# Kernel optimization log

Hardware: AMD Instinct MI355X
Metric: run time of the kernel (lower is better)

The kernel has to match this reference:

```python
import jax, jax.numpy as jnp
import numpy as np

N = 50000
E = 800000
F_IN = 300
ALPHA = 0.5                      # GCN2Conv alpha
BETA = float(np.log(0.2 / 2.0 + 1.0))  # log(theta/layer + 1), theta=0.2, layer=2
NEG_SLOPE = 0.2                  # GATv2 leaky_relu slope
H, DH = 2, 32                    # GATv2 heads, per-head dim


def _glorot(key, shape):
    s = (6.0 / (shape[0] + shape[-1])) ** 0.5
    return jax.random.uniform(key, shape, jnp.float32, -s, s)


def setup_inputs() -> dict:
    key = jax.random.key(0)
    ks = jax.random.split(key, 24)
    inp = {
        'x': jax.random.normal(ks[0], (N, F_IN), jnp.float32),
        'edge_index': jax.random.randint(ks[1], (2, E), 0, N, dtype=jnp.int32),
        # encoder params
        'W_enc1': _glorot(ks[2], (F_IN, 256)), 'b_enc1': jnp.zeros((256,), jnp.float32),
        'W_enc2': _glorot(ks[3], (256, 256)),                       # GCN2Conv (no bias)
        'W_enc3': _glorot(ks[4], (256, 128)), 'b_enc3': jnp.zeros((128,), jnp.float32),
        'W_enc4': _glorot(ks[5], (128, 64)),  'b_enc4': jnp.zeros((64,), jnp.float32),
        'W_enc5': _glorot(ks[6], (64, 32)),   'b_enc5': jnp.zeros((32,), jnp.float32),
        'Wl_gat': _glorot(ks[7], (32, H * DH)),
        'Wr_gat': _glorot(ks[8], (32, H * DH)),
        'att_gat': _glorot(ks[9], (H, DH)),
        'b_gat': jnp.zeros((H * DH,), jnp.float32),
        # decoder params
        'W_dec1': _glorot(ks[10], (64, 128)),  'b_dec1': jnp.zeros((128,), jnp.float32),
        'W_dec2': _glorot(ks[11], (128, 256)), 'b_dec2': jnp.zeros((256,), jnp.float32),
        'W_dec3': _glorot(ks[12], (256, 256)),                      # GCN2Conv (no bias)
        'W_dec4': _glorot(ks[13], (256, F_IN)), 'b_dec4': jnp.zeros((F_IN,), jnp.float32),
    }
    return inp


def _forward(x, edge_index,
             W_enc1, b_enc1, W_enc2, W_enc3, b_enc3, W_enc4, b_enc4, W_enc5, b_enc5,
             Wl_gat, Wr_gat, att_gat, b_gat,
             W_dec1, b_dec1, W_dec2, b_dec2, W_dec3, W_dec4, b_dec4):
    loops = jnp.arange(N, dtype=edge_index.dtype)
    src = jnp.concatenate([edge_index[0], loops])  # [E+N]
    dst = jnp.concatenate([edge_index[1], loops])
    # symmetric GCN normalization with self-loops (PyG gcn_norm)
    deg = jax.ops.segment_sum(jnp.ones_like(src, jnp.float32), dst, num_segments=N)
    dinv = jnp.where(deg > 0, jax.lax.rsqrt(jnp.maximum(deg, 1e-12)), 0.0)
    norm = dinv[src] * dinv[dst]  # [E+N]

    def prop(h):  # normalized adjacency apply: gather -> scale -> scatter-add
        return jax.ops.segment_sum(h[src] * norm[:, None], dst, num_segments=N)

    def gcn(h, W, b):
        return prop(h @ W) + b

    def gcn2(h, W):  # GCNII with x_0 = layer input, shared weights
        hp = (1.0 - ALPHA) * prop(h) + ALPHA * h
        return (1.0 - BETA) * hp + BETA * (hp @ W)

    def gatv2(h, Wl, Wr, att, b):
        xl = (h @ Wl).reshape(N, H, DH)  # source transform
        xr = (h @ Wr).reshape(N, H, DH)  # target transform
        e = jax.nn.leaky_relu(xl[src] + xr[dst], NEG_SLOPE)  # [E+N, H, DH]
        logits = jnp.einsum('ehd,hd->eh', e, att)            # [E+N, H]
        m = jax.lax.stop_gradient(jax.ops.segment_max(logits, dst, num_segments=N))
        ex = jnp.exp(logits - m[dst])
        den = jax.ops.segment_sum(ex, dst, num_segments=N)
        a = ex / (den[dst] + 1e-16)                          # softmax over in-edges
        out = jax.ops.segment_sum(xl[src] * a[:, :, None], dst, num_segments=N)
        return out.reshape(N, H * DH) + b

    h = gcn(x, W_enc1, b_enc1)
    h = gcn2(h, W_enc2)
    h = gcn(h, W_enc3, b_enc3)
    h = gcn(h, W_enc4, b_enc4)
    h = gcn(h, W_enc5, b_enc5)
    h = gatv2(h, Wl_gat, Wr_gat, att_gat, b_gat)
    h = jax.nn.relu(h)
    h = gcn(h, W_dec1, b_dec1)
    h = gcn(h, W_dec2, b_dec2)
    h = gcn2(h, W_dec3)
    h = gcn(h, W_dec4, b_dec4)
    return jax.nn.sigmoid(h)


def reference(x, edge_index,
              W_enc1, b_enc1, W_enc2, W_enc3, b_enc3, W_enc4, b_enc4, W_enc5, b_enc5,
              Wl_gat, Wr_gat, att_gat, b_gat,
              W_dec1, b_dec1, W_dec2, b_dec2, W_dec3, W_dec4, b_dec4):
    return _forward(x, edge_index,
                    W_enc1, b_enc1, W_enc2, W_enc3, b_enc3, W_enc4, b_enc4, W_enc5, b_enc5,
                    Wl_gat, Wr_gat, att_gat, b_gat,
                    W_dec1, b_dec1, W_dec2, b_dec2, W_dec3, W_dec4, b_dec4)
```

## Files before the change

### kernel.cpp

```cpp
#include <hip/hip_runtime.h>
#include <math.h>

#define NN 50000
#define FIN 300
#define SS 304
constexpr float ALPHA_C = 0.5f;
constexpr float BETA_C  = 0.09531017980432486f;
constexpr float NEG_SLOPE = 0.2f;

typedef unsigned short u16;
typedef __attribute__((ext_vector_type(8))) short short8;
typedef __attribute__((ext_vector_type(4))) float f32x4;
typedef _Float16 hf4 __attribute__((ext_vector_type(4)));

__global__ void hist_kernel(const int* __restrict__ dst, int* __restrict__ deg, int E) {
    int e = blockIdx.x * blockDim.x + threadIdx.x;
    if (e < E) atomicAdd(&deg[dst[e]], 1);
}

__global__ void scan_kernel(const int* __restrict__ deg, int* __restrict__ rowptr, int n) {
    __shared__ int sh[1024];
    __shared__ int carry;
    if (threadIdx.x == 0) { carry = 0; rowptr[0] = 0; }
    __syncthreads();
    for (int base = 0; base < n; base += 1024) {
        int i = base + threadIdx.x;
        int v = (i < n) ? deg[i] : 0;
        sh[threadIdx.x] = v;
        __syncthreads();
        for (int off = 1; off < 1024; off <<= 1) {
            int t = (threadIdx.x >= off) ? sh[threadIdx.x - off] : 0;
            __syncthreads();
            sh[threadIdx.x] += t;
            __syncthreads();
        }
        if (i < n) rowptr[i + 1] = sh[threadIdx.x] + carry;
        __syncthreads();
        if (threadIdx.x == 0) carry += sh[1023];
        __syncthreads();
    }
}

__global__ void dinv_kernel(const int* __restrict__ deg, float* __restrict__ dinv, int n) {
    int i = blockIdx.x * blockDim.x + threadIdx.x;
    if (i < n) dinv[i] = rsqrtf((float)deg[i] + 1.0f);
}

__global__ void copy_int_kernel(const int* __restrict__ a, int* __restrict__ b, int n) {
    int i = blockIdx.x * blockDim.x + threadIdx.x;
    if (i < n) b[i] = a[i];
}

__global__ void fill_kernel(const int* __restrict__ src, const int* __restrict__ dst,
                            const float* __restrict__ dinv, int* __restrict__ cursor,
                            int* __restrict__ csr_src, float* __restrict__ csr_w, int E) {
    int e = blockIdx.x * blockDim.x + threadIdx.x;
    if (e < E) {
        int s = src[e], d = dst[e];
        int p = atomicAdd(&cursor[d], 1);
        csr_src[p] = s;
        csr_w[p]   = dinv[s] * dinv[d];
    }
}

__global__ void splitw_kernel(const float* __restrict__ W, u16* __restrict__ WhT,
                              u16* __restrict__ WlT, int K, int M, int Kp, int total) {
    int t = blockIdx.x * blockDim.x + threadIdx.x;
    if (t >= total) return;
    int c = t / Kp, k = t - c * Kp;
    float x = (c < M && k < K) ? W[(size_t)k * M + c] : 0.f;
    unsigned u = __float_as_uint(x);
    WhT[t] = (u16)(u >> 16);
    float lo = x - __uint_as_float(u & 0xFFFF0000u);
    WlT[t] = (u16)(__float_as_uint(lo) >> 16);
}

__global__ __launch_bounds__(256)
void gemm_mfma_kernel(const float* __restrict__ A, const u16* __restrict__ WhT,
                      const u16* __restrict__ WlT, float* __restrict__ C,
                      _Float16* __restrict__ Cs, int n, int K, int M, int Kp,
                      float cAB, float cA, const float* __restrict__ bias, int gx) {
    __shared__ u16 sAh[64 * 40], sAl[64 * 40], sWh[64 * 40], sWl[64 * 40];
    const int tid = threadIdx.x;
    const int nwg = gridDim.x;
    const int q = nwg >> 3, r = nwg & 7;
    const int xcd = blockIdx.x & 7, off = blockIdx.x >> 3;
    const int wgid = (xcd < r ? xcd * (q + 1) : r * (q + 1) + (xcd - r) * q) + off;
    const int colBase = (wgid % gx) * 64;
    const int rowBase = (wgid / gx) * 64;
    const int lane = tid & 63, wid = tid >> 6;
    const int wr = (wid >> 1) * 32, wc = (wid & 1) * 32;
    const int fr = lane & 15, ko = (lane >> 4) * 8;
    const int wsc = tid >> 2, wsk = (tid & 3) * 8;

    f32x4 acc[2][2] = {};

    for (int k0 = 0; k0 < Kp; k0 += 32) {
        {
            size_t g = (size_t)(colBase + wsc) * Kp + k0 + wsk;
            *(uint4*)&sWh[wsc * 40 + wsk] = *(const uint4*)&WhT[g];
            *(uint4*)&sWl[wsc * 40 + wsk] = *(const uint4*)&WlT[g];
        }
        const bool fullk = (k0 + 32 <= K);
        for (int s = tid; s < 512; s += 256) {
            int rr = s >> 3, kb = (s & 7) * 4;
            int gr = rowBase + rr, kk = k0 + kb;
            float x0 = 0.f, x1 = 0.f, x2 = 0.f, x3 = 0.f;
            if (gr < n) {
                const float* ap = A + (size_t)gr * K + kk;
                if (fullk) { float4 v = *(const float4*)ap; x0 = v.x; x1 = v.y; x2 = v.z; x3 = v.w; }
                else {
                    if (kk     < K) x0 = ap[0];
                    if (kk + 1 < K) x1 = ap[1];
                    if (kk + 2 < K) x2 = ap[2];
                    if (kk + 3 < K) x3 = ap[3];
                }
            }
            unsigned u0 = __float_as_uint(x0), u1 = __float_as_uint(x1);
            unsigned u2 = __float_as_uint(x2), u3 = __float_as_uint(x3);
            uint2 hp; hp.x = (u1 & 0xFFFF0000u) | (u0 >> 16);
                      hp.y = (u3 & 0xFFFF0000u) | (u2 >> 16);
            float l0 = x0 - __uint_as_float(u0 & 0xFFFF0000u);
            float l1 = x1 - __uint_as_float(u1 & 0xFFFF0000u);
            float l2 = x2 - __uint_as_float(u2 & 0xFFFF0000u);
            float l3 = x3 - __uint_as_float(u3 & 0xFFFF0000u);
            uint2 lp; lp.x = (__float_as_uint(l1) & 0xFFFF0000u) | (__float_as_uint(l0) >> 16);
                      lp.y = (__float_as_uint(l3) & 0xFFFF0000u) | (__float_as_uint(l2) >> 16);
            *(uint2*)&sAh[rr * 40 + kb] = hp;
            *(uint2*)&sAl[rr * 40 + kb] = lp;
        }
        __syncthreads();

        short8 ah[2], al[2], bh[2], bl[2];
        ah[0] = *(const short8*)&sAh[(wr +      fr) * 40 + ko];
        ah[1] = *(const short8*)&sAh[(wr + 16 + fr) * 40 + ko];
        al[0] = *(const short8*)&sAl[(wr +      fr) * 40 + ko];
        al[1] = *(const short8*)&sAl[(wr + 16 + fr) * 40 + ko];
        bh[0] = *(const short8*)&sWh[(wc +      fr) * 40 + ko];
        bh[1] = *(const short8*)&sWh[(wc + 16 + fr) * 40 + ko];
        bl[0] = *(const short8*)&sWl[(wc +      fr) * 40 + ko];
        bl[1] = *(const short8*)&sWl[(wc + 16 + fr) * 40 + ko];
#pragma unroll
        for (int i = 0; i < 2; i++)
#pragma unroll
            for (int j = 0; j < 2; j++) {
                acc[i][j] = __builtin_amdgcn_mfma_f32_16x16x32_bf16(al[i], bh[j], acc[i][j], 0, 0, 0);
                acc[i][j] = __builtin_amdgcn_mfma_f32_16x16x32_bf16(ah[i], bl[j], acc[i][j], 0, 0, 0);
                acc[i][j] = __builtin_amdgcn_mfma_f32_16x16x32_bf16(ah[i], bh[j], acc[i][j], 0, 0, 0);
            }
        __syncthreads();
    }

#pragma unroll
    for (int i = 0; i < 2; i++)
#pragma unroll
        for (int j = 0; j < 2; j++) {
            int row0 = rowBase + wr + i * 16 + (lane >> 4) * 4;
            int col  = colBase + wc + j * 16 + fr;
            if (col >= M) continue;
            float bv = bias ? bias[col] : 0.f;
#pragma unroll
            for (int qq = 0; qq < 4; qq++) {
                int rr = row0 + qq;
                if (rr >= n) break;
                float v = cAB * acc[i][j][qq] + bv;
                if (cA != 0.f) v += cA * A[(size_t)rr * K + col];
                C[(size_t)rr * M + col] = v;
                if (Cs) Cs[(size_t)rr * SS + col] = (_Float16)v;
            }
        }
}

__global__ __launch_bounds__(256)
void prop_kernel(const float* __restrict__ h, const _Float16* __restrict__ hs,
                 float* __restrict__ out, _Float16* __restrict__ outs,
                 const int* __restrict__ rowptr, const int* __restrict__ csr_src,
                 const float* __restrict__ csr_w, const float* __restrict__ dinv,
                 const float* __restrict__ bias, int n, int D, float cP, float cH) {
    int wv = (blockIdx.x * blockDim.x + threadIdx.x) >> 6;
    int lane = threadIdx.x & 63;
    int D4 = D >> 2;
    int npw = 64 / D4;
    int sub = lane / D4;
    int cl = lane - sub * D4;
    int i = wv * npw + sub;
    if (i >= n) return;
    int c = cl * 4;
    long bi = (long)i * D4 + cl;
    const float4* h4 = (const float4*)h;
    float4 hv = h4[bi];
    float sw = dinv[i] * dinv[i];
    float4 a0 = {sw * hv.x, sw * hv.y, sw * hv.z, sw * hv.w};
    float4 a1 = {0,0,0,0}, a2 = {0,0,0,0}, a3 = {0,0,0,0};
    int p0 = rowptr[i], p1 = rowptr[i + 1];
    int p = p0;
    for (; p + 4 <= p1; p += 4) {
        int s0 = csr_src[p], s1 = csr_src[p+1], s2 = csr_src[p+2], s3 = csr_src[p+3];
        float w0 = csr_w[p], w1 = csr_w[p+1], w2 = csr_w[p+2], w3 = csr_w[p+3];
        hf4 v0 = *(const hf4*)&hs[(size_t)s0 * SS + c];
        hf4 v1 = *(const hf4*)&hs[(size_t)s1 * SS + c];
        hf4 v2 = *(const hf4*)&hs[(size_t)s2 * SS + c];
        hf4 v3 = *(const hf4*)&hs[(size_t)s3 * SS + c];
        a0.x += w0*(float)v0[0]; a0.y += w0*(float)v0[1]; a0.z += w0*(float)v0[2]; a0.w += w0*(float)v0[3];
        a1.x += w1*(float)v1[0]; a1.y += w1*(float)v1[1]; a1.z += w1*(float)v1[2]; a1.w += w1*(float)v1[3];
        a2.x += w2*(float)v2[0]; a2.y += w2*(float)v2[1]; a2.z += w2*(float)v2[2]; a2.w += w2*(float)v2[3];
        a3.x += w3*(float)v3[0]; a3.y += w3*(float)v3[1]; a3.z += w3*(float)v3[2]; a3.w += w3*(float)v3[3];
    }
    for (; p < p1; ++p) {
        int s = csr_src[p];
        float w = csr_w[p];
        hf4 v = *(const hf4*)&hs[(size_t)s * SS + c];
        a0.x += w*(float)v[0]; a0.y += w*(float)v[1]; a0.z += w*(float)v[2]; a0.w += w*(float)v[3];
    }
    float4 acc = {a0.x + a1.x + a2.x + a3.x, a0.y + a1.y + a2.y + a3.y,
                  a0.z + a1.z + a2.z + a3.z, a0.w + a1.w + a2.w + a3.w};
    float4 rr = {cP * acc.x, cP * acc.y, cP * acc.z, cP * acc.w};
    if (cH != 0.f) { rr.x += cH * hv.x; rr.y += cH * hv.y; rr.z += cH * hv.z; rr.w += cH * hv.w; }
    if (bias) { float4 b = ((const float4*)bias)[cl]; rr.x += b.x; rr.y += b.y; rr.z += b.z; rr.w += b.w; }
    ((float4*)out)[bi] = rr;
    if (outs) {
        hf4 o; o[0] = (_Float16)rr.x; o[1] = (_Float16)rr.y; o[2] = (_Float16)rr.z; o[3] = (_Float16)rr.w;
        *(hf4*)&outs[(size_t)i * SS + c] = o;
    }
}

__device__ inline float lrelu(float x) { return x > 0.f ? x : NEG_SLOPE * x; }

__global__ __launch_bounds__(256)
void gat_logits_kernel(const float* __restrict__ xl, const _Float16* __restrict__ xls,
                       const float* __restrict__ xr, const float* __restrict__ att,
                       const int* __restrict__ rowptr, const int* __restrict__ csr_src,
                       float* __restrict__ logits, float* __restrict__ self_logits, int n) {
    int t = blockIdx.x * blockDim.x + threadIdx.x;
    int i = t >> 1, hh = t & 1;
    if (i >= n) return;
    float4 attv[8], xrv[8];
    const float4* att4 = (const float4*)att;
    const float4* xr4 = (const float4*)xr;
#pragma unroll
    for (int c = 0; c < 8; c++) {
        attv[c] = att4[hh * 8 + c];
        xrv[c]  = xr4[(long)i * 16 + hh * 8 + c];
    }
    {
        const float4* xl4 = (const float4*)xl;
        float s = 0.f;
        long b = (long)i * 16 + hh * 8;
#pragma unroll
        for (int c = 0; c < 8; c++) {
            float4 e = xl4[b + c];
            s += lrelu(e.x + xrv[c].x) * attv[c].x;
            s += lrelu(e.y + xrv[c].y) * attv[c].y;
            s += lrelu(e.z + xrv[c].z) * attv[c].z;
            s += lrelu(e.w + xrv[c].w) * attv[c].w;
        }
        self_logits[i * 2 + hh] = s;
    }
    int p0 = rowptr[i], p1 = rowptr[i + 1];
    for (int p = p0; p < p1; ++p) {
        int sn = csr_src[p];
        size_t b = (size_t)sn * SS + hh * 32;
        float s = 0.f;
#pragma unroll
        for (int c = 0; c < 8; c++) {
            hf4 e = *(const hf4*)&xls[b + c * 4];
            s += lrelu((float)e[0] + xrv[c].x) * attv[c].x;
            s += lrelu((float)e[1] + xrv[c].y) * attv[c].y;
            s += lrelu((float)e[2] + xrv[c].z) * attv[c].z;
            s += lrelu((float)e[3] + xrv[c].w) * attv[c].w;
        }
        logits[(long)p * 2 + hh] = s;
    }
}

__global__ __launch_bounds__(256)
void gat_mden_kernel(const float* __restrict__ logits, const float* __restrict__ self_logits,
                     const int* __restrict__ rowptr, float* __restrict__ m_arr,
                     float* __restrict__ den_arr, int n) {
    int t = blockIdx.x * blockDim.x + threadIdx.x;
    int i = t >> 1, hh = t & 1;
    if (i >= n) return;
    int p0 = rowptr[i], p1 = rowptr[i + 1];
    float m = self_logits[i * 2 + hh];
    for (int p = p0; p < p1; ++p) m = fmaxf(m, logits[(long)p * 2 + hh]);
    float den = expf(self_logits[i * 2 + hh] - m);
    for (int p = p0; p < p1; ++p) den += expf(logits[(long)p * 2 + hh] - m);
    m_arr[i * 2 + hh] = m;
    den_arr[i * 2 + hh] = den;
}

__global__ __launch_bounds__(256)
void gat_out_kernel(const float* __restrict__ xl, const _Float16* __restrict__ xls,
                    const int* __restrict__ rowptr, const int* __restrict__ csr_src,
                    const float* __restrict__ logits, const float* __restrict__ self_logits,
                    const float* __restrict__ m_arr, const float* __restrict__ den_arr,
                    const float* __restrict__ bias, float* __restrict__ out,
                    _Float16* __restrict__ outs, int n) {
    int i = (blockIdx.x * blockDim.x + threadIdx.x) >> 6;
    int lane = threadIdx.x & 63;
    if (i >= n) return;
    int hh = lane >> 5;
    float m = m_arr[i * 2 + hh];
    float inv = 1.f / (den_arr[i * 2 + hh] + 1e-16f);
    float acc = expf(self_logits[i * 2 + hh] - m) * inv * xl[(long)i * 64 + lane];
    int p0 = rowptr[i], p1 = rowptr[i + 1];
    for (int p = p0; p < p1; ++p) {
        float w = expf(logits[(long)p * 2 + hh] - m) * inv;
        acc += w * (float)xls[(size_t)csr_src[p] * SS + lane];
    }
    float r = fmaxf(acc + bias[lane], 0.f);
    out[(long)i * 64 + lane] = r;
    outs[(size_t)i * SS + lane] = (_Float16)r;
}

__global__ void sigmoid_kernel(const float* __restrict__ in, float* __restrict__ out, int n4) {
    int i = blockIdx.x * blockDim.x + threadIdx.x;
    if (i < n4) {
        float4 v = ((const float4*)in)[i];
        float4 r;
        r.x = 1.f / (1.f + expf(-v.x));
        r.y = 1.f / (1.f + expf(-v.y));
        r.z = 1.f / (1.f + expf(-v.z));
        r.w = 1.f / (1.f + expf(-v.w));
        ((float4*)out)[i] = r;
    }
}

extern "C" void kernel_launch(void* const* d_in, const int* in_sizes, int n_in,
                              void* d_out, int out_size, void* d_ws, size_t ws_size,
                              hipStream_t stream) {
    const int N = NN;
    const int E = in_sizes[1] / 2;

    struct WSpec { int idx; int K, M; };
    const WSpec wspec[11] = {
        {2, 300, 256},
        {4, 256, 256},
        {5, 256, 128},
        {7, 128, 64},
        {9, 64, 32},
        {11, 32, 64},
        {12, 32, 64},
        {15, 64, 128},
        {17, 128, 256},
        {19, 256, 256},
        {20, 256, 300},
    };
    size_t arena_elems = 0;
    int kp[11], mp[11];
    size_t woff[11];
    for (int i = 0; i < 11; i++) {
        kp[i] = (wspec[i].K + 31) & ~31;
        mp[i] = (wspec[i].M + 63) & ~63;
        woff[i] = arena_elems;
        arena_elems += (size_t)2 * mp[i] * kp[i];
    }

    size_t need = 0;
    need += (size_t)N * 304 * 4 * 2;
    need += (size_t)N * SS * 2;
    need += (size_t)E * 4;
    need += (size_t)E * 2 * 4;
    need += (size_t)N * 2 * 4 * 3;
    need += (size_t)N * 4;
    need += (size_t)N * 4;
    need += (size_t)(N + 4) * 4;
    need += (size_t)N * 4;
    need += (size_t)E * 4;
    need += arena_elems * 2 + 128;
    if (ws_size < need) return;

    const float* x      = (const float*)d_in[0];
    const int*   ei     = (const int*)d_in[1];
    const int*   e_src  = ei;
    const int*   e_dst  = ei + E;
    const float* b1  = (const float*)d_in[3];
    const float* b3  = (const float*)d_in[6];
    const float* b4  = (const float*)d_in[8];
    const float* b5  = (const float*)d_in[10];
    const float* attw= (const float*)d_in[13];
    const float* bg  = (const float*)d_in[14];
    const float* bd1 = (const float*)d_in[16];
    const float* bd2 = (const float*)d_in[18];
    const float* bd4 = (const float*)d_in[21];

    char* w = (char*)d_ws;
    float* bufA = (float*)w;                 w += (size_t)N * 304 * 4;
    float* bufB = (float*)w;                 w += (size_t)N * 304 * 4;
    _Float16* S = (_Float16*)w;              w += (size_t)N * SS * 2;
    float* csr_w = (float*)w;                w += (size_t)E * 4;
    float* logits = (float*)w;               w += (size_t)E * 2 * 4;
    float* self_logits = (float*)w;          w += (size_t)N * 2 * 4;
    float* m_arr = (float*)w;                w += (size_t)N * 2 * 4;
    float* den_arr = (float*)w;              w += (size_t)N * 2 * 4;
    float* dinv = (float*)w;                 w += (size_t)N * 4;
    int* deg = (int*)w;                      w += (size_t)N * 4;
    int* rowptr = (int*)w;                   w += (size_t)(N + 4) * 4;
    int* cursor = (int*)w;                   w += (size_t)N * 4;
    int* csr_src = (int*)w;                  w += (size_t)E * 4;
    w = (char*)(((size_t)w + 63) & ~(size_t)63);
    u16* arena = (u16*)w;                    w += arena_elems * 2;
    float* T = (float*)d_out;

    int nb_e = (E + 255) / 256;
    int nb_n = (N + 255) / 256;
    int nb_wave = (N + 3) / 4;
    int nb_2n = (2 * N + 255) / 256;

    for (int i = 0; i < 11; i++) {
        int total = mp[i] * kp[i];
        splitw_kernel<<<(total + 255) / 256, 256, 0, stream>>>(
            (const float*)d_in[wspec[i].idx], arena + woff[i], arena + woff[i] + total,
            wspec[i].K, wspec[i].M, kp[i], total);
    }

    hipMemsetAsync(deg, 0, (size_t)N * 4, stream);
    hist_kernel<<<nb_e, 256, 0, stream>>>(e_dst, deg, E);
    scan_kernel<<<1, 1024, 0, stream>>>(deg, rowptr, N);
    dinv_kernel<<<nb_n, 256, 0, stream>>>(deg, dinv, N);
    copy_int_kernel<<<nb_n, 256, 0, stream>>>(rowptr, cursor, N);
    fill_kernel<<<nb_e, 256, 0, stream>>>(e_src, e_dst, dinv, cursor, csr_src, csr_w, E);

    auto gemm = [&](int wi, const float* A, float* C, float cAB, float cA,
                    const float* bias, bool shadow) {
        int K = wspec[wi].K, M = wspec[wi].M;
        int total = mp[wi] * kp[wi];
        int gx = (M + 63) / 64, gy = (N + 63) / 64;
        gemm_mfma_kernel<<<gx * gy, 256, 0, stream>>>(
            A, arena + woff[wi], arena + woff[wi] + total, C, shadow ? S : nullptr,
            N, K, M, kp[wi], cAB, cA, bias, gx);
    };
    auto prop = [&](const float* h, float* out, int D, float cP, float cH,
                    const float* bias, bool shadow) {
        int npw = 64 / (D >> 2);
        int npb = 4 * npw;
        int nb = (N + npb - 1) / npb;
        prop_kernel<<<nb, 256, 0, stream>>>(h, S, out, shadow ? S : nullptr,
                                            rowptr, csr_src, csr_w, dinv,
                                            bias, N, D, cP, cH);
    };

    gemm(0, x, T, 1.f, 0.f, nullptr, true);
    prop(T, bufA, 256, 1.f, 0.f, b1, true);
    prop(bufA, bufB, 256, 1.f - ALPHA_C, ALPHA_C, nullptr, false);
    gemm(1, bufB, bufA, BETA_C, 1.f - BETA_C, nullptr, false);
    gemm(2, bufA, T, 1.f, 0.f, nullptr, true);
    prop(T, bufB, 128, 1.f, 0.f, b3, false);
    gemm(3, bufB, T, 1.f, 0.f, nullptr, true);
    prop(T, bufA, 64, 1.f, 0.f, b4, false);
    gemm(4, bufA, T, 1.f, 0.f, nullptr, true);
    prop(T, bufB, 32, 1.f, 0.f, b5, false);
    gemm(5, bufB, bufA, 1.f, 0.f, nullptr, true);
    gemm(6, bufB, T, 1.f, 0.f, nullptr, false);
    gat_logits_kernel<<<nb_2n, 256, 0, stream>>>(bufA, S, T, attw, rowptr, csr_src,
                                                 logits, self_logits, N);
    gat_mden_kernel<<<nb_2n, 256, 0, stream>>>(logits, self_logits, rowptr, m_arr, den_arr, N);
    gat_out_kernel<<<nb_wave, 256, 0, stream>>>(bufA, S, rowptr, csr_src, logits, self_logits,
                                                m_arr, den_arr, bg, bufB, S, N);
    prop(bufB, bufA, 64, 1.f, 0.f, nullptr, false);
    gemm(7, bufA, T, 1.f, 0.f, bd1, true);
    prop(T, bufB, 128, 1.f, 0.f, nullptr, false);
    gemm(8, bufB, bufA, 1.f, 0.f, bd2, true);
    prop(bufA, bufB, 256, 1.f - ALPHA_C, ALPHA_C, nullptr, false);
    gemm(9, bufB, bufA, BETA_C, 1.f - BETA_C, nullptr, true);
    prop(bufA, bufB, 256, 1.f, 0.f, nullptr, false);
    gemm(10, bufB, T, 1.f, 0.f, bd4, false);
    sigmoid_kernel<<<(out_size / 4 + 255) / 256, 256, 0, stream>>>(T, (float*)d_out, out_size / 4);
}
```

Measured before the change: 1.326 ms.

## Switch activations to fp16 storage and use split-weight f16 MFMA GEMMs

```diff
diff --git a/kernel.cpp b/kernel.cpp
--- a/kernel.cpp
+++ b/kernel.cpp
@@ -3,15 +3,16 @@
 
 #define NN 50000
 #define FIN 300
-#define SS 304
+#define SHS 256
+#define XS  320
 constexpr float ALPHA_C = 0.5f;
 constexpr float BETA_C  = 0.09531017980432486f;
 constexpr float NEG_SLOPE = 0.2f;
 
 typedef unsigned short u16;
-typedef __attribute__((ext_vector_type(8))) short short8;
 typedef __attribute__((ext_vector_type(4))) float f32x4;
 typedef _Float16 hf4 __attribute__((ext_vector_type(4)));
+typedef _Float16 half8 __attribute__((ext_vector_type(8)));
 
 __global__ void hist_kernel(const int* __restrict__ dst, int* __restrict__ deg, int E) {
     int e = blockIdx.x * blockDim.x + threadIdx.x;
@@ -63,24 +64,31 @@
     }
 }
 
-__global__ void splitw_kernel(const float* __restrict__ W, u16* __restrict__ WhT,
-                              u16* __restrict__ WlT, int K, int M, int Kp, int total) {
+__global__ void cvt_x_kernel(const float* __restrict__ x, _Float16* __restrict__ FX, int total) {
+    int t = blockIdx.x * blockDim.x + threadIdx.x;
+    if (t >= total) return;
+    int i = t / XS, c = t - i * XS;
+    FX[t] = (c < FIN) ? (_Float16)x[(size_t)i * FIN + c] : (_Float16)0.f;
+}
+
+__global__ void splitw_kernel(const float* __restrict__ W, _Float16* __restrict__ WhT,
+                              _Float16* __restrict__ WlT, int K, int M, int Kp, int total) {
     int t = blockIdx.x * blockDim.x + threadIdx.x;
     if (t >= total) return;
     int c = t / Kp, k = t - c * Kp;
     float x = (c < M && k < K) ? W[(size_t)k * M + c] : 0.f;
-    unsigned u = __float_as_uint(x);
-    WhT[t] = (u16)(u >> 16);
-    float lo = x - __uint_as_float(u & 0xFFFF0000u);
-    WlT[t] = (u16)(__float_as_uint(lo) >> 16);
+    _Float16 hi = (_Float16)x;
+    WhT[t] = hi;
+    WlT[t] = (_Float16)(x - (float)hi);
 }
 
 __global__ __launch_bounds__(256)
-void gemm_mfma_kernel(const float* __restrict__ A, const u16* __restrict__ WhT,
-                      const u16* __restrict__ WlT, float* __restrict__ C,
-                      _Float16* __restrict__ Cs, int n, int K, int M, int Kp,
-                      float cAB, float cA, const float* __restrict__ bias, int gx) {
-    __shared__ u16 sAh[64 * 40], sAl[64 * 40], sWh[64 * 40], sWl[64 * 40];
+void gemm_f16_kernel(const _Float16* __restrict__ A, int lda,
+                     const _Float16* __restrict__ WhT, const _Float16* __restrict__ WlT,
+                     float* __restrict__ Cf, _Float16* __restrict__ Co,
+                     int n, int Kl, int M,
+                     float cAB, float cA, const float* __restrict__ bias, int gx) {
+    __shared__ _Float16 sA[64 * 40], sWh[64 * 40], sWl[64 * 40];
     const int tid = threadIdx.x;
     const int nwg = gridDim.x;
     const int q = nwg >> 3, r = nwg & 7;
@@ -92,61 +100,37 @@
     const int wr = (wid >> 1) * 32, wc = (wid & 1) * 32;
     const int fr = lane & 15, ko = (lane >> 4) * 8;
     const int wsc = tid >> 2, wsk = (tid & 3) * 8;
+    const int arr = tid >> 2, akq = (tid & 3) * 8;
 
     f32x4 acc[2][2] = {};
 
-    for (int k0 = 0; k0 < Kp; k0 += 32) {
+    for (int k0 = 0; k0 < Kl; k0 += 32) {
         {
-            size_t g = (size_t)(colBase + wsc) * Kp + k0 + wsk;
+            size_t g = (size_t)(colBase + wsc) * Kl + k0 + wsk;
             *(uint4*)&sWh[wsc * 40 + wsk] = *(const uint4*)&WhT[g];
             *(uint4*)&sWl[wsc * 40 + wsk] = *(const uint4*)&WlT[g];
         }
-        const bool fullk = (k0 + 32 <= K);
-        for (int s = tid; s < 512; s += 256) {
-            int rr = s >> 3, kb = (s & 7) * 4;
-            int gr = rowBase + rr, kk = k0 + kb;
-            float x0 = 0.f, x1 = 0.f, x2 = 0.f, x3 = 0.f;
-            if (gr < n) {
-                const float* ap = A + (size_t)gr * K + kk;
-                if (fullk) { float4 v = *(const float4*)ap; x0 = v.x; x1 = v.y; x2 = v.z; x3 = v.w; }
-                else {
-                    if (kk     < K) x0 = ap[0];
-                    if (kk + 1 < K) x1 = ap[1];
-                    if (kk + 2 < K) x2 = ap[2];
-                    if (kk + 3 < K) x3 = ap[3];
-                }
-            }
-            unsigned u0 = __float_as_uint(x0), u1 = __float_as_uint(x1);
-            unsigned u2 = __float_as_uint(x2), u3 = __float_as_uint(x3);
-            uint2 hp; hp.x = (u1 & 0xFFFF0000u) | (u0 >> 16);
-                      hp.y = (u3 & 0xFFFF0000u) | (u2 >> 16);
-            float l0 = x0 - __uint_as_float(u0 & 0xFFFF0000u);
-            float l1 = x1 - __uint_as_float(u1 & 0xFFFF0000u);
-            float l2 = x2 - __uint_as_float(u2 & 0xFFFF0000u);
-            float l3 = x3 - __uint_as_float(u3 & 0xFFFF0000u);
-            uint2 lp; lp.x = (__float_as_uint(l1) & 0xFFFF0000u) | (__float_as_uint(l0) >> 16);
-                      lp.y = (__float_as_uint(l3) & 0xFFFF0000u) | (__float_as_uint(l2) >> 16);
-            *(uint2*)&sAh[rr * 40 + kb] = hp;
-            *(uint2*)&sAl[rr * 40 + kb] = lp;
+        {
+            int gr = rowBase + arr;
+            uint4 v = {0, 0, 0, 0};
+            if (gr < n) v = *(const uint4*)&A[(size_t)gr * lda + k0 + akq];
+            *(uint4*)&sA[arr * 40 + akq] = v;
         }
         __syncthreads();
 
-        short8 ah[2], al[2], bh[2], bl[2];
-        ah[0] = *(const short8*)&sAh[(wr +      fr) * 40 + ko];
-        ah[1] = *(const short8*)&sAh[(wr + 16 + fr) * 40 + ko];
-        al[0] = *(const short8*)&sAl[(wr +      fr) * 40 + ko];
-        al[1] = *(const short8*)&sAl[(wr + 16 + fr) * 40 + ko];
-        bh[0] = *(const short8*)&sWh[(wc +      fr) * 40 + ko];
-        bh[1] = *(const short8*)&sWh[(wc + 16 + fr) * 40 + ko];
-        bl[0] = *(const short8*)&sWl[(wc +      fr) * 40 + ko];
-        bl[1] = *(const short8*)&sWl[(wc + 16 + fr) * 40 + ko];
+        half8 av[2], bh[2], bl[2];
+        av[0] = *(const half8*)&sA[(wr +      fr) * 40 + ko];
+        av[1] = *(const half8*)&sA[(wr + 16 + fr) * 40 + ko];
+        bh[0] = *(const half8*)&sWh[(wc +      fr) * 40 + ko];
+        bh[1] = *(const half8*)&sWh[(wc + 16 + fr) * 40 + ko];
+        bl[0] = *(const half8*)&sWl[(wc +      fr) * 40 + ko];
+        bl[1] = *(const half8*)&sWl[(wc + 16 + fr) * 40 + ko];
 #pragma unroll
         for (int i = 0; i < 2; i++)
 #pragma unroll
             for (int j = 0; j < 2; j++) {
-                acc[i][j] = __builtin_amdgcn_mfma_f32_16x16x32_bf16(al[i], bh[j], acc[i][j], 0, 0, 0);
-                acc[i][j] = __builtin_amdgcn_mfma_f32_16x16x32_bf16(ah[i], bl[j], acc[i][j], 0, 0, 0);
-                acc[i][j] = __builtin_amdgcn_mfma_f32_16x16x32_bf16(ah[i], bh[j], acc[i][j], 0, 0, 0);
+                acc[i][j] = __builtin_amdgcn_mfma_f32_16x16x32_f16(av[i], bl[j], acc[i][j], 0, 0, 0);
+                acc[i][j] = __builtin_amdgcn_mfma_f32_16x16x32_f16(av[i], bh[j], acc[i][j], 0, 0, 0);
             }
         __syncthreads();
     }
@@ -164,16 +148,15 @@
                 int rr = row0 + qq;
                 if (rr >= n) break;
                 float v = cAB * acc[i][j][qq] + bv;
-                if (cA != 0.f) v += cA * A[(size_t)rr * K + col];
-                C[(size_t)rr * M + col] = v;
-                if (Cs) Cs[(size_t)rr * SS + col] = (_Float16)v;
+                if (cA != 0.f) v += cA * (float)A[(size_t)rr * lda + col];
+                if (Cf) Cf[(size_t)rr * M + col] = v;
+                if (Co) Co[(size_t)rr * SHS + col] = (_Float16)v;
             }
         }
 }
 
 __global__ __launch_bounds__(256)
-void prop_kernel(const float* __restrict__ h, const _Float16* __restrict__ hs,
-                 float* __restrict__ out, _Float16* __restrict__ outs,
+void prop_kernel(const _Float16* __restrict__ Fin, _Float16* __restrict__ Fout,
                  const int* __restrict__ rowptr, const int* __restrict__ csr_src,
                  const float* __restrict__ csr_w, const float* __restrict__ dinv,
                  const float* __restrict__ bias, int n, int D, float cP, float cH) {
@@ -186,9 +169,8 @@
     int i = wv * npw + sub;
     if (i >= n) return;
     int c = cl * 4;
-    long bi = (long)i * D4 + cl;
-    const float4* h4 = (const float4*)h;
-    float4 hv = h4[bi];
+    hf4 th = *(const hf4*)&Fin[(size_t)i * SHS + c];
+    float4 hv = {(float)th[0], (float)th[1], (float)th[2], (float)th[3]};
     float sw = dinv[i] * dinv[i];
     float4 a0 = {sw * hv.x, sw * hv.y, sw * hv.z, sw * hv.w};
     float4 a1 = {0,0,0,0}, a2 = {0,0,0,0}, a3 = {0,0,0,0};
@@ -197,10 +179,10 @@
     for (; p + 4 <= p1; p += 4) {
         int s0 = csr_src[p], s1 = csr_src[p+1], s2 = csr_src[p+2], s3 = csr_src[p+3];
         float w0 = csr_w[p], w1 = csr_w[p+1], w2 = csr_w[p+2], w3 = csr_w[p+3];
-        hf4 v0 = *(const hf4*)&hs[(size_t)s0 * SS + c];
-        hf4 v1 = *(const hf4*)&hs[(size_t)s1 * SS + c];
-        hf4 v2 = *(const hf4*)&hs[(size_t)s2 * SS + c];
-        hf4 v3 = *(const hf4*)&hs[(size_t)s3 * SS + c];
+        hf4 v0 = *(const hf4*)&Fin[(size_t)s0 * SHS + c];
+        hf4 v1 = *(const hf4*)&Fin[(size_t)s1 * SHS + c];
+        hf4 v2 = *(const hf4*)&Fin[(size_t)s2 * SHS + c];
+        hf4 v3 = *(const hf4*)&Fin[(size_t)s3 * SHS + c];
         a0.x += w0*(float)v0[0]; a0.y += w0*(float)v0[1]; a0.z += w0*(float)v0[2]; a0.w += w0*(float)v0[3];
         a1.x += w1*(float)v1[0]; a1.y += w1*(float)v1[1]; a1.z += w1*(float)v1[2]; a1.w += w1*(float)v1[3];
         a2.x += w2*(float)v2[0]; a2.y += w2*(float)v2[1]; a2.z += w2*(float)v2[2]; a2.w += w2*(float)v2[3];
@@ -209,7 +191,7 @@
     for (; p < p1; ++p) {
         int s = csr_src[p];
         float w = csr_w[p];
-        hf4 v = *(const hf4*)&hs[(size_t)s * SS + c];
+        hf4 v = *(const hf4*)&Fin[(size_t)s * SHS + c];
         a0.x += w*(float)v[0]; a0.y += w*(float)v[1]; a0.z += w*(float)v[2]; a0.w += w*(float)v[3];
     }
     float4 acc = {a0.x + a1.x + a2.x + a3.x, a0.y + a1.y + a2.y + a3.y,
@@ -217,20 +199,17 @@
     float4 rr = {cP * acc.x, cP * acc.y, cP * acc.z, cP * acc.w};
     if (cH != 0.f) { rr.x += cH * hv.x; rr.y += cH * hv.y; rr.z += cH * hv.z; rr.w += cH * hv.w; }
     if (bias) { float4 b = ((const float4*)bias)[cl]; rr.x += b.x; rr.y += b.y; rr.z += b.z; rr.w += b.w; }
-    ((float4*)out)[bi] = rr;
-    if (outs) {
-        hf4 o; o[0] = (_Float16)rr.x; o[1] = (_Float16)rr.y; o[2] = (_Float16)rr.z; o[3] = (_Float16)rr.w;
-        *(hf4*)&outs[(size_t)i * SS + c] = o;
-    }
+    hf4 o; o[0] = (_Float16)rr.x; o[1] = (_Float16)rr.y; o[2] = (_Float16)rr.z; o[3] = (_Float16)rr.w;
+    *(hf4*)&Fout[(size_t)i * SHS + c] = o;
 }
 
 __device__ inline float lrelu(float x) { return x > 0.f ? x : NEG_SLOPE * x; }
 
 __global__ __launch_bounds__(256)
-void gat_logits_kernel(const float* __restrict__ xl, const _Float16* __restrict__ xls,
-                       const float* __restrict__ xr, const float* __restrict__ att,
-                       const int* __restrict__ rowptr, const int* __restrict__ csr_src,
-                       float* __restrict__ logits, float* __restrict__ self_logits, int n) {
+void gat_logits_kernel(const _Float16* __restrict__ xl, const float* __restrict__ xr,
+                       const float* __restrict__ att, const int* __restrict__ rowptr,
+                       const int* __restrict__ csr_src, float* __restrict__ logits,
+                       float* __restrict__ self_logits, int n) {
     int t = blockIdx.x * blockDim.x + threadIdx.x;
     int i = t >> 1, hh = t & 1;
     if (i >= n) return;
@@ -243,27 +222,26 @@
         xrv[c]  = xr4[(long)i * 16 + hh * 8 + c];
     }
     {
-        const float4* xl4 = (const float4*)xl;
         float s = 0.f;
-        long b = (long)i * 16 + hh * 8;
+        size_t b = (size_t)i * SHS + hh * 32;
 #pragma unroll
         for (int c = 0; c < 8; c++) {
-            float4 e = xl4[b + c];
-            s += lrelu(e.x + xrv[c].x) * attv[c].x;
-            s += lrelu(e.y + xrv[c].y) * attv[c].y;
-            s += lrelu(e.z + xrv[c].z) * attv[c].z;
-            s += lrelu(e.w + xrv[c].w) * attv[c].w;
+            hf4 e = *(const hf4*)&xl[b + c * 4];
+            s += lrelu((float)e[0] + xrv[c].x) * attv[c].x;
+            s += lrelu((float)e[1] + xrv[c].y) * attv[c].y;
+            s += lrelu((float)e[2] + xrv[c].z) * attv[c].z;
+            s += lrelu((float)e[3] + xrv[c].w) * attv[c].w;
         }
         self_logits[i * 2 + hh] = s;
     }
     int p0 = rowptr[i], p1 = rowptr[i + 1];
     for (int p = p0; p < p1; ++p) {
         int sn = csr_src[p];
-        size_t b = (size_t)sn * SS + hh * 32;
+        size_t b = (size_t)sn * SHS + hh * 32;
         float s = 0.f;
 #pragma unroll
         for (int c = 0; c < 8; c++) {
-            hf4 e = *(const hf4*)&xls[b + c * 4];
+            hf4 e = *(const hf4*)&xl[b + c * 4];
             s += lrelu((float)e[0] + xrv[c].x) * attv[c].x;
             s += lrelu((float)e[1] + xrv[c].y) * attv[c].y;
             s += lrelu((float)e[2] + xrv[c].z) * attv[c].z;
@@ -290,27 +268,25 @@
 }
 
 __global__ __launch_bounds__(256)
-void gat_out_kernel(const float* __restrict__ xl, const _Float16* __restrict__ xls,
-                    const int* __restrict__ rowptr, const int* __restrict__ csr_src,
-                    const float* __restrict__ logits, const float* __restrict__ self_logits,
-                    const float* __restrict__ m_arr, const float* __restrict__ den_arr,
-                    const float* __restrict__ bias, float* __restrict__ out,
-                    _Float16* __restrict__ outs, int n) {
+void gat_out_kernel(const _Float16* __restrict__ xl, const int* __restrict__ rowptr,
+                    const int* __restrict__ csr_src, const float* __restrict__ logits,
+                    const float* __restrict__ self_logits, const float* __restrict__ m_arr,
+                    const float* __restrict__ den_arr, const float* __restrict__ bias,
+                    _Float16* __restrict__ Fout, int n) {
     int i = (blockIdx.x * blockDim.x + threadIdx.x) >> 6;
     int lane = threadIdx.x & 63;
     if (i >= n) return;
     int hh = lane >> 5;
     float m = m_arr[i * 2 + hh];
     float inv = 1.f / (den_arr[i * 2 + hh] + 1e-16f);
-    float acc = expf(self_logits[i * 2 + hh] - m) * inv * xl[(long)i * 64 + lane];
+    float acc = expf(self_logits[i * 2 + hh] - m) * inv * (float)xl[(size_t)i * SHS + lane];
     int p0 = rowptr[i], p1 = rowptr[i + 1];
     for (int p = p0; p < p1; ++p) {
         float w = expf(logits[(long)p * 2 + hh] - m) * inv;
-        acc += w * (float)xls[(size_t)csr_src[p] * SS + lane];
+        acc += w * (float)xl[(size_t)csr_src[p] * SHS + lane];
     }
     float r = fmaxf(acc + bias[lane], 0.f);
-    out[(long)i * 64 + lane] = r;
-    outs[(size_t)i * SS + lane] = (_Float16)r;
+    Fout[(size_t)i * SHS + lane] = (_Float16)r;
 }
 
 __global__ void sigmoid_kernel(const float* __restrict__ in, float* __restrict__ out, int n4) {
@@ -357,15 +333,13 @@
     }
 
     size_t need = 0;
-    need += (size_t)N * 304 * 4 * 2;
-    need += (size_t)N * SS * 2;
+    need += (size_t)N * XS * 2;
+    need += (size_t)N * SHS * 2 * 2;
     need += (size_t)E * 4;
     need += (size_t)E * 2 * 4;
     need += (size_t)N * 2 * 4 * 3;
-    need += (size_t)N * 4;
-    need += (size_t)N * 4;
+    need += (size_t)N * 4 * 3;
     need += (size_t)(N + 4) * 4;
-    need += (size_t)N * 4;
     need += (size_t)E * 4;
     need += arena_elems * 2 + 128;
     if (ws_size < need) return;
@@ -385,9 +359,9 @@
     const float* bd4 = (const float*)d_in[21];
 
     char* w = (char*)d_ws;
-    float* bufA = (float*)w;                 w += (size_t)N * 304 * 4;
-    float* bufB = (float*)w;                 w += (size_t)N * 304 * 4;
-    _Float16* S = (_Float16*)w;              w += (size_t)N * SS * 2;
+    _Float16* FX = (_Float16*)w;             w += (size_t)N * XS * 2;
+    _Float16* F0 = (_Float16*)w;             w += (size_t)N * SHS * 2;
+    _Float16* F1 = (_Float16*)w;             w += (size_t)N * SHS * 2;
     float* csr_w = (float*)w;                w += (size_t)E * 4;
     float* logits = (float*)w;               w += (size_t)E * 2 * 4;
     float* self_logits = (float*)w;          w += (size_t)N * 2 * 4;
@@ -399,7 +373,7 @@
     int* cursor = (int*)w;                   w += (size_t)N * 4;
     int* csr_src = (int*)w;                  w += (size_t)E * 4;
     w = (char*)(((size_t)w + 63) & ~(size_t)63);
-    u16* arena = (u16*)w;                    w += arena_elems * 2;
+    _Float16* arena = (_Float16*)w;          w += arena_elems * 2;
     float* T = (float*)d_out;
 
     int nb_e = (E + 255) / 256;
@@ -413,6 +387,7 @@
             (const float*)d_in[wspec[i].idx], arena + woff[i], arena + woff[i] + total,
             wspec[i].K, wspec[i].M, kp[i], total);
     }
+    cvt_x_kernel<<<((N * XS) + 255) / 256, 256, 0, stream>>>(x, FX, N * XS);
 
     hipMemsetAsync(deg, 0, (size_t)N * 4, stream);
     hist_kernel<<<nb_e, 256, 0, stream>>>(e_dst, deg, E);
@@ -421,49 +396,49 @@
     copy_int_kernel<<<nb_n, 256, 0, stream>>>(rowptr, cursor, N);
     fill_kernel<<<nb_e, 256, 0, stream>>>(e_src, e_dst, dinv, cursor, csr_src, csr_w, E);
 
-    auto gemm = [&](int wi, const float* A, float* C, float cAB, float cA,
-                    const float* bias, bool shadow) {
-        int K = wspec[wi].K, M = wspec[wi].M;
+    auto gemm = [&](int wi, const _Float16* A, int lda, float* Cf, _Float16* Co,
+                    float cAB, float cA, const float* bias) {
+        int M = wspec[wi].M;
+        int Kl = kp[wi];
         int total = mp[wi] * kp[wi];
         int gx = (M + 63) / 64, gy = (N + 63) / 64;
-        gemm_mfma_kernel<<<gx * gy, 256, 0, stream>>>(
-            A, arena + woff[wi], arena + woff[wi] + total, C, shadow ? S : nullptr,
-            N, K, M, kp[wi], cAB, cA, bias, gx);
+        gemm_f16_kernel<<<gx * gy, 256, 0, stream>>>(
+            A, lda, arena + woff[wi], arena + woff[wi] + total,
+            Cf, Co, N, Kl, M, cAB, cA, bias, gx);
     };
-    auto prop = [&](const float* h, float* out, int D, float cP, float cH,
-                    const float* bias, bool shadow) {
+    auto prop = [&](const _Float16* Fin, _Float16* Fout, int D, float cP, float cH,
+                    const float* bias) {
         int npw = 64 / (D >> 2);
         int npb = 4 * npw;
         int nb = (N + npb - 1) / npb;
-        prop_kernel<<<nb, 256, 0, stream>>>(h, S, out, shadow ? S : nullptr,
-                                            rowptr, csr_src, csr_w, dinv,
+        prop_kernel<<<nb, 256, 0, stream>>>(Fin, Fout, rowptr, csr_src, csr_w, dinv,
                                             bias, N, D, cP, cH);
     };
 
-    gemm(0, x, T, 1.f, 0.f, nullptr, true);
-    prop(T, bufA, 256, 1.f, 0.f, b1, true);
-    prop(bufA, bufB, 256, 1.f - ALPHA_C, ALPHA_C, nullptr, false);
-    gemm(1, bufB, bufA, BETA_C, 1.f - BETA_C, nullptr, false);
-    gemm(2, bufA, T, 1.f, 0.f, nullptr, true);
-    prop(T, bufB, 128, 1.f, 0.f, b3, false);
-    gemm(3, bufB, T, 1.f, 0.f, nullptr, true);
-    prop(T, bufA, 64, 1.f, 0.f, b4, false);
-    gemm(4, bufA, T, 1.f, 0.f, nullptr, true);
-    prop(T, bufB, 32, 1.f, 0.f, b5, false);
-    gemm(5, bufB, bufA, 1.f, 0.f, nullptr, true);
-    gemm(6, bufB, T, 1.f, 0.f, nullptr, false);
-    gat_logits_kernel<<<nb_2n, 256, 0, stream>>>(bufA, S, T, attw, rowptr, csr_src,
+    gemm(0, FX, XS, nullptr, F0, 1.f, 0.f, nullptr);
+    prop(F0, F1, 256, 1.f, 0.f, b1);
+    prop(F1, F0, 256, 1.f - ALPHA_C, ALPHA_C, nullptr);
+    gemm(1, F0, SHS, nullptr, F1, BETA_C, 1.f - BETA_C, nullptr);
+    gemm(2, F1, SHS, nullptr, F0, 1.f, 0.f, nullptr);
+    prop(F0, F1, 128, 1.f, 0.f, b3);
+    gemm(3, F1, SHS, nullptr, F0, 1.f, 0.f, nullptr);
+    prop(F0, F1, 64, 1.f, 0.f, b4);
+    gemm(4, F1, SHS, nullptr, F0, 1.f, 0.f, nullptr);
+    prop(F0, F1, 32, 1.f, 0.f, b5);
+    gemm(5, F1, SHS, nullptr, F0, 1.f, 0.f, nullptr);
+    gemm(6, F1, SHS, T, nullptr, 1.f, 0.f, nullptr);
+    gat_logits_kernel<<<nb_2n, 256, 0, stream>>>(F0, T, attw, rowptr, csr_src,
                                                  logits, self_logits, N);
     gat_mden_kernel<<<nb_2n, 256, 0, stream>>>(logits, self_logits, rowptr, m_arr, den_arr, N);
-    gat_out_kernel<<<nb_wave, 256, 0, stream>>>(bufA, S, rowptr, csr_src, logits, self_logits,
-                                                m_arr, den_arr, bg, bufB, S, N);
-    prop(bufB, bufA, 64, 1.f, 0.f, nullptr, false);
-    gemm(7, bufA, T, 1.f, 0.f, bd1, true);
-    prop(T, bufB, 128, 1.f, 0.f, nullptr, false);
-    gemm(8, bufB, bufA, 1.f, 0.f, bd2, true);
-    prop(bufA, bufB, 256, 1.f - ALPHA_C, ALPHA_C, nullptr, false);
-    gemm(9, bufB, bufA, BETA_C, 1.f - BETA_C, nullptr, true);
-    prop(bufA, bufB, 256, 1.f, 0.f, nullptr, false);
-    gemm(10, bufB, T, 1.f, 0.f, bd4, false);
+    gat_out_kernel<<<nb_wave, 256, 0, stream>>>(F0, rowptr, csr_src, logits, self_logits,
+                                                m_arr, den_arr, bg, F1, N);
+    prop(F1, F0, 64, 1.f, 0.f, nullptr);
+    gemm(7, F0, SHS, nullptr, F1, 1.f, 0.f, bd1);
+    prop(F1, F0, 128, 1.f, 0.f, nullptr);
+    gemm(8, F0, SHS, nullptr, F1, 1.f, 0.f, bd2);
+    prop(F1, F0, 256, 1.f - ALPHA_C, ALPHA_C, nullptr);
+    gemm(9, F0, SHS, nullptr, F1, BETA_C, 1.f - BETA_C, nullptr);
+    prop(F1, F0, 256, 1.f, 0.f, nullptr);
+    gemm(10, F0, SHS, T, nullptr, 1.f, 0.f, bd4);
     sigmoid_kernel<<<(out_size / 4 + 255) / 256, 256, 0, stream>>>(T, (float*)d_out, out_size / 4);
 }
```

Measured after the change: 1.089 ms. -17.9%, faster.
